# Performance work log

Hardware: AMD Instinct MI355X
Metric: run time of the kernel (lower is better)

The kernel has to match this reference:

```python
import jax, jax.numpy as jnp
import numpy as np

D_MODEL = 512
STATE = 128
HALF = STATE // 2
SEQ = 4096
BATCH = 8


def setup_inputs() -> dict:
    key = jax.random.key(0)
    ks = jax.random.split(key, 4)
    u = jax.random.normal(ks[0], (BATCH, SEQ, D_MODEL), dtype=jnp.float32)
    # HiPPO init: Lambda = -0.5 + i*pi*n, n=1..HALF
    n = jnp.arange(1, HALF + 1, dtype=jnp.float32)
    log_Lambda_real = jnp.log(jnp.full((HALF,), 0.5, dtype=jnp.float32))  # log(-real) with real=-0.5
    Lambda_imag = jnp.pi * n
    B_real = jnp.ones((HALF, D_MODEL), dtype=jnp.float32)
    B_imag = jnp.zeros((HALF, D_MODEL), dtype=jnp.float32)
    C_real = jax.random.normal(ks[1], (D_MODEL, HALF), dtype=jnp.float32) / np.sqrt(STATE)
    C_imag = jax.random.normal(ks[2], (D_MODEL, HALF), dtype=jnp.float32) / np.sqrt(STATE)
    D = jax.random.normal(ks[3], (D_MODEL, D_MODEL), dtype=jnp.float32) / np.sqrt(D_MODEL)
    log_Delta = jnp.array([-3.0], dtype=jnp.float32)
    return {
        "u": u,
        "log_Lambda_real": log_Lambda_real,
        "Lambda_imag": Lambda_imag,
        "B_real": B_real,
        "B_imag": B_imag,
        "C_real": C_real,
        "C_imag": C_imag,
        "D": D,
        "log_Delta": log_Delta,
    }


def reference(u, log_Lambda_real, Lambda_imag, B_real, B_imag, C_real, C_imag, D, log_Delta):
    T = u.shape[1]
    Bc = B_real + 1j * B_imag            # (N/2, P) complex
    Cc = C_real + 1j * C_imag            # (P, N/2) complex
    # --- bilinear (Tustin) discretization ---
    Delta = jnp.exp(log_Delta)           # (1,)
    Lambda = -jnp.exp(jnp.clip(log_Lambda_real, -10.0, 10.0)) + 1j * Lambda_imag  # (N/2,)
    denom = 1.0 - (Delta / 2.0) * Lambda
    A_bar = (1.0 + (Delta / 2.0) * Lambda) / denom          # (N/2,)
    B_bar = (Delta / denom)[:, None] * Bc                   # (N/2, P)
    # --- FFT convolution with the SSM kernel k[n,t] = A_bar[n]^t ---
    t_idx = jnp.arange(T)
    k = jnp.exp(jnp.log(A_bar)[:, None] * t_idx[None, :])   # (N/2, T)
    u_c = u.astype(jnp.complex64)
    v = jnp.einsum('np,btp->bnt', B_bar, u_c)               # (B, N/2, T)
    fft_size = 2 * T
    V_f = jnp.fft.fft(v, n=fft_size, axis=-1)
    K_f = jnp.fft.fft(k, n=fft_size, axis=-1)
    conv = jnp.fft.ifft(V_f * K_f[None, :, :], axis=-1)[..., :T]  # (B, N/2, T)
    y = 2.0 * jnp.einsum('pn,bnt->btp', Cc, conv).real      # (B, T, P)
    return y + u @ D.T
```

## Files before the change

### kernel.cpp

```cpp
#include <hip/hip_runtime.h>
#include <hip/hip_bf16.h>
#include <stdint.h>


#define BATCH 8
#define SEQ   4096
#define DMODEL 512
#define HALF  64
#define CHUNK 64
#define NCHUNK (SEQ / CHUNK)
#define NT    10

typedef __attribute__((ext_vector_type(8))) short short8;
typedef __attribute__((ext_vector_type(4))) float f32x4;

__device__ __forceinline__ unsigned short f2bf(float f) {
    unsigned int u = __float_as_uint(f);
    u += 0x7fffu + ((u >> 16) & 1u);
    return (unsigned short)(u >> 16);
}
__device__ __forceinline__ float bf2f(unsigned short s) {
    return __uint_as_float((unsigned)s << 16);
}

__device__ __forceinline__ void poleA(const float* logLr, const float* Li_in,
                                      const float* logDelta, int n,
                                      float& Ar, float& Ai) {
    float Delta = expf(logDelta[0]);
    float llr = fminf(fmaxf(logLr[n], -10.f), 10.f);
    float Lr = -expf(llr);
    float Li = Li_in[n];
    float dr = 1.f - 0.5f * Delta * Lr;
    float di = -0.5f * Delta * Li;
    float dn = dr * dr + di * di;
    float nr = 1.f + 0.5f * Delta * Lr;
    float ni = 0.5f * Delta * Li;
    Ar = (nr * dr + ni * di) / dn;
    Ai = (ni * dr - nr * di) / dn;
}

#define GLOAD_LDS16(g, l)                                                    \
    __builtin_amdgcn_global_load_lds(                                        \
        (const __attribute__((address_space(1))) unsigned int*)(g),          \
        (__attribute__((address_space(3))) unsigned int*)(l), 16, 0, 0)

__global__ void k_build(const float* __restrict__ logLr, const float* __restrict__ Li_in,
                        const float* __restrict__ logDelta,
                        const float* __restrict__ Br, const float* __restrict__ Bi,
                        const float* __restrict__ Cr, const float* __restrict__ Ci,
                        const float* __restrict__ D,
                        unsigned short* __restrict__ Mv, unsigned short* __restrict__ W) {
    int bid = blockIdx.x;
    if (bid < 128) {
        int np = bid, p = threadIdx.x;
        if (p < DMODEL) {
            int n = np & 63;
            float Delta = expf(logDelta[0]);
            float llr = fminf(fmaxf(logLr[n], -10.f), 10.f);
            float Lr = -expf(llr);
            float Li = Li_in[n];
            float dr = 1.f - 0.5f * Delta * Lr;
            float di = -0.5f * Delta * Li;
            float dn = dr * dr + di * di;
            float sr = Delta * dr / dn;
            float si = -Delta * di / dn;
            float br = Br[n * DMODEL + p], bi = Bi[n * DMODEL + p];
            float v = (np < HALF) ? (sr * br - si * bi) : (si * br + sr * bi);
            Mv[np * DMODEL + p] = f2bf(v);
        }
    } else {
        int p = bid - 128, j = threadIdx.x;
        float v;
        if (j < HALF) v = 2.f * Cr[p * HALF + j];
        else if (j < 2 * HALF) v = -2.f * Ci[p * HALF + (j - HALF)];
        else v = D[p * DMODEL + (j - 2 * HALF)];
        W[p * 640 + j] = f2bf(v);
    }
}

__global__ void k_scanA(const unsigned short* __restrict__ Vb,
                        const float* __restrict__ logLr, const float* __restrict__ Li_in,
                        const float* __restrict__ logDelta,
                        float* __restrict__ E) {
    int tid = threadIdx.x;
    int n = tid & 63;
    int c = ((blockIdx.x & 31) << 1) + (tid >> 6);
    int b = blockIdx.x >> 5;
    float Ar, Ai;
    poleA(logLr, Li_in, logDelta, n, Ar, Ai);
    float xr = 0.f, xi = 0.f;
    size_t base = ((size_t)b * SEQ + (size_t)c * CHUNK) * 128 + n;
    for (int tl = 0; tl < CHUNK; ++tl) {
        float vr = bf2f(Vb[base]), vi = bf2f(Vb[base + 64]);
        float nxr = Ar * xr - Ai * xi + vr;
        float nxi = Ar * xi + Ai * xr + vi;
        xr = nxr; xi = nxi;
        base += 128;
    }
    int eidx = ((b * NCHUNK + c) * 2) * HALF + n;
    E[eidx] = xr; E[eidx + 64] = xi;
}

__global__ void k_scanCB(const unsigned short* __restrict__ Vb,
                         const float* __restrict__ E,
                         const float* __restrict__ logLr, const float* __restrict__ Li_in,
                         const float* __restrict__ logDelta,
                         unsigned short* __restrict__ Xb) {
    int tid = threadIdx.x;
    int n = tid & 63;
    int c = ((blockIdx.x & 31) << 1) + (tid >> 6);
    int b = blockIdx.x >> 5;
    float Ar, Ai;
    poleA(logLr, Li_in, logDelta, n, Ar, Ai);
    float a64r = Ar, a64i = Ai;
#pragma unroll
    for (int s = 0; s < 6; ++s) {
        float t = a64r * a64r - a64i * a64i;
        a64i = 2.f * a64r * a64i;
        a64r = t;
    }
    float xr = 0.f, xi = 0.f, wr = 1.f, wi = 0.f;
    for (int jj = 1; jj <= c; ++jj) {
        int ei = ((b * NCHUNK + (c - jj)) * 2) * HALF + n;
        float er = E[ei], ev = E[ei + 64];
        xr += wr * er - wi * ev;
        xi += wr * ev + wi * er;
        float nwr = wr * a64r - wi * a64i;
        float nwi = wr * a64i + wi * a64r;
        wr = nwr; wi = nwi;
    }
    size_t base = ((size_t)b * SEQ + (size_t)c * CHUNK) * 128 + n;
    for (int tl = 0; tl < CHUNK; ++tl) {
        float vr = bf2f(Vb[base]), vi = bf2f(Vb[base + 64]);
        float nxr = Ar * xr - Ai * xi + vr;
        float nxi = Ar * xi + Ai * xr + vi;
        xr = nxr; xi = nxi;
        Xb[base] = f2bf(xr); Xb[base + 64] = f2bf(xi);
        base += 128;
    }
}

__global__ __launch_bounds__(512) void gemm1(const float* __restrict__ U,
                                             const unsigned short* __restrict__ Mv,
                                             unsigned short* __restrict__ Vb,
                                             unsigned short* __restrict__ Ub) {
    __shared__ __align__(16) unsigned short As[64 * 32];
    __shared__ __align__(16) unsigned short Bs[128 * 32];
    const int tid = threadIdx.x;
    const int lane = tid & 63;
    const int w = tid >> 6;
    const int wm = w >> 2, wn = w & 3;
    const int l15 = lane & 15, l4 = lane >> 4;
    const int row0 = blockIdx.x * 64;
    const int srow = tid >> 3;
    const int sh = (tid & 7) * 4;

    f32x4 acc[2][2];
#pragma unroll
    for (int m = 0; m < 2; ++m)
#pragma unroll
        for (int n = 0; n < 2; ++n) acc[m][n] = (f32x4)(0.f);

    for (int k0 = 0; k0 < DMODEL; k0 += 32) {
        const float4 av = *(const float4*)(U + (size_t)(row0 + srow) * DMODEL + k0 + sh);

        __syncthreads();

        GLOAD_LDS16(Mv + (size_t)(tid >> 2) * DMODEL + k0 + (tid & 3) * 8,
                    &Bs[(w * 64) * 8]);

        uint2 wa;
        wa.x = (unsigned)f2bf(av.x) | ((unsigned)f2bf(av.y) << 16);
        wa.y = (unsigned)f2bf(av.z) | ((unsigned)f2bf(av.w) << 16);
        *(uint2*)&As[srow * 32 + sh] = wa;
        *(uint2*)&Ub[(size_t)(row0 + srow) * DMODEL + k0 + sh] = wa;

        __syncthreads();

        short8 af[2], bf[2];
#pragma unroll
        for (int m = 0; m < 2; ++m)
            af[m] = *(const short8*)&As[(wm * 32 + m * 16 + l15) * 32 + l4 * 8];
#pragma unroll
        for (int n = 0; n < 2; ++n)
            bf[n] = *(const short8*)&Bs[(wn * 32 + n * 16 + l15) * 32 + l4 * 8];
#pragma unroll
        for (int m = 0; m < 2; ++m)
#pragma unroll
            for (int n = 0; n < 2; ++n)
                acc[m][n] = __builtin_amdgcn_mfma_f32_16x16x32_bf16(af[m], bf[n], acc[m][n], 0, 0, 0);
    }

#pragma unroll
    for (int m = 0; m < 2; ++m) {
        int rbase = row0 + wm * 32 + m * 16 + l4 * 4;
#pragma unroll
        for (int n = 0; n < 2; ++n) {
            int col = wn * 32 + n * 16 + l15;
#pragma unroll
            for (int r = 0; r < 4; ++r)
                Vb[(size_t)(rbase + r) * 128 + col] = f2bf(acc[m][n][r]);
        }
    }
}


#define STAGE_K(t, kh, j) do {                                                 \
    int c_ = (kh) * 1024 + (j) * 512 + tid;                                    \
    int ct_ = c_ ^ (((c_ >> 5) & 1) << 1);                                     \
    int r_ = (ct_ >> 2) & 255;                                                 \
    int kcol_ = (t) * 64 + (kh) * 32 + (ct_ & 3) * 8;                          \
    const unsigned short* asrc_ = (kcol_ < 128)                                \
        ? Xb + (size_t)(row0 + r_) * 128 + kcol_                               \
        : Ub + (size_t)(row0 + r_) * 512 + (kcol_ - 128);                      \
    GLOAD_LDS16(asrc_, &As[((t) & 1) * 16384 + ((kh) * 1024 + (j) * 512 + w * 64) * 8]); \
    GLOAD_LDS16(W + (size_t)(col0 + r_) * 640 + kcol_,                         \
                &Bs[((t) & 1) * 16384 + ((kh) * 1024 + (j) * 512 + w * 64) * 8]); \
} while (0)

#define LDAB(t, kh) do {                                                       \
    _Pragma("unroll") for (int i_ = 0; i_ < 8; ++i_) {                         \
        int r_ = wm * 128 + i_ * 16 + l15;                                     \
        int c_ = (l4 * 8) ^ (((r_ >> 3) & 1) << 4);                            \
        af[i_] = *(const short8*)&As[((t) & 1) * 16384 + (kh) * 8192 + r_ * 32 + c_]; \
    }                                                                          \
    _Pragma("unroll") for (int j_ = 0; j_ < 4; ++j_) {                         \
        int r_ = wn * 64 + j_ * 16 + l15;                                      \
        int c_ = (l4 * 8) ^ (((r_ >> 3) & 1) << 4);                            \
        bf[j_] = *(const short8*)&Bs[((t) & 1) * 16384 + (kh) * 8192 + r_ * 32 + c_]; \
    } } while (0)

#define MFMA32() do {                                                          \
    __builtin_amdgcn_s_setprio(1);                                             \
    _Pragma("unroll") for (int i_ = 0; i_ < 8; ++i_)                           \
    _Pragma("unroll") for (int j_ = 0; j_ < 4; ++j_)                           \
        acc[i_][j_] = __builtin_amdgcn_mfma_f32_16x16x32_bf16(                 \
            bf[j_], af[i_], acc[i_][j_], 0, 0, 0);                             \
    __builtin_amdgcn_s_setprio(0);                                             \
} while (0)

#define PHASE_SYNC(N) do {                                                     \
    asm volatile("s_waitcnt vmcnt(" #N ")" ::: "memory");                      \
    __builtin_amdgcn_s_barrier();                                              \
    __builtin_amdgcn_sched_barrier(0);                                         \
} while (0)

__global__ __launch_bounds__(512) void gemm23_8p(const unsigned short* __restrict__ Xb,
                                                 const unsigned short* __restrict__ Ub,
                                                 const unsigned short* __restrict__ W,
                                                 float* __restrict__ C) {
    __shared__ __align__(16) unsigned short As[2 * 16384];
    __shared__ __align__(16) unsigned short Bs[2 * 16384];
    const int tid = threadIdx.x;
    const int lane = tid & 63;
    const int w = tid >> 6;
    const int wm = w >> 2, wn = w & 3;
    const int l15 = lane & 15, l4 = lane >> 4;

    int lin = blockIdx.y * gridDim.x + blockIdx.x;
    int sw = (lin & 7) * 32 + (lin >> 3);
    const int row0 = (sw & 127) * 256;
    const int col0 = (sw >> 7) * 256;

    f32x4 acc[8][4];
#pragma unroll
    for (int m = 0; m < 8; ++m)
#pragma unroll
        for (int n = 0; n < 4; ++n) acc[m][n] = (f32x4)(0.f);

    STAGE_K(0, 0, 0); STAGE_K(0, 0, 1);
    STAGE_K(0, 1, 0); STAGE_K(0, 1, 1);
    STAGE_K(1, 0, 0); STAGE_K(1, 0, 1);

    short8 af[8], bf[4];
    for (int t = 0; t < NT - 1; ++t) {
        PHASE_SYNC(8);
        LDAB(t, 0);
        STAGE_K(t + 1, 1, 0); STAGE_K(t + 1, 1, 1);
        MFMA32();
        PHASE_SYNC(8);
        LDAB(t, 1);
        if (t < NT - 2) { STAGE_K(t + 2, 0, 0); STAGE_K(t + 2, 0, 1); }
        MFMA32();
    }
    PHASE_SYNC(4);
    LDAB(NT - 1, 0);
    MFMA32();
    PHASE_SYNC(0);
    LDAB(NT - 1, 1);
    MFMA32();

#pragma unroll
    for (int i = 0; i < 8; ++i) {
        int row = row0 + wm * 128 + i * 16 + l15;
#pragma unroll
        for (int j = 0; j < 4; ++j) {
            int col = col0 + wn * 64 + j * 16 + l4 * 4;
            *(float4*)&C[(size_t)row * DMODEL + col] =
                make_float4(acc[i][j][0], acc[i][j][1], acc[i][j][2], acc[i][j][3]);
        }
    }
}


extern "C" void kernel_launch(void* const* d_in, const int* in_sizes, int n_in,
                              void* d_out, int out_size, void* d_ws, size_t ws_size,
                              hipStream_t stream) {
    const float* u      = (const float*)d_in[0];
    const float* logLr  = (const float*)d_in[1];
    const float* Li     = (const float*)d_in[2];
    const float* Br     = (const float*)d_in[3];
    const float* Bi     = (const float*)d_in[4];
    const float* Cr     = (const float*)d_in[5];
    const float* Ci     = (const float*)d_in[6];
    const float* D      = (const float*)d_in[7];
    const float* logDel = (const float*)d_in[8];
    float* out = (float*)d_out;

    const size_t M = (size_t)BATCH * SEQ;
    unsigned short* Vb = (unsigned short*)d_ws;
    unsigned short* Ub = Vb + M * 128;
    unsigned short* Xb = Ub + M * 512;
    unsigned short* Mv = Xb + M * 128;
    unsigned short* W  = Mv + 128 * 512;
    float* E     = (float*)(W + 512 * 640);

    hipLaunchKernelGGL(k_build, dim3(640), dim3(640), 0, stream,
                       logLr, Li, logDel, Br, Bi, Cr, Ci, D, Mv, W);

    hipLaunchKernelGGL(gemm1, dim3(M / 64), dim3(512), 0, stream, u, Mv, Vb, Ub);

    hipLaunchKernelGGL(k_scanA, dim3(256), dim3(128), 0, stream,
                       Vb, logLr, Li, logDel, E);
    hipLaunchKernelGGL(k_scanCB, dim3(256), dim3(128), 0, stream,
                       Vb, E, logLr, Li, logDel, Xb);

    hipLaunchKernelGGL(gemm23_8p, dim3(M / 256, DMODEL / 256), dim3(512), 0, stream,
                       Xb, Ub, W, out);
}
```

Measured before the change: 79.82 us.

## Fuse chunk-end scan state computation into gemm1 epilogue

Removes the separate k_scanA kernel. The per-chunk final state is now computed inside gemm1's epilogue as a weighted sum of the fp32 accumulators times powers of the pole A (A^(63-t)), reduced with wave shuffles and shared memory. This saves one kernel launch and a full sequential re-read of Vb. The trade is extra epilogue math, a block sync in gemm1, and a closed-form power sum in place of the sequential recurrence, which may shift rounding (it now uses fp32 accumulators rather than bf16 Vb).

New measurement: 78.24 us, median of 3. -2.0%, faster.

```diff
diff --git a/kernel.cpp b/kernel.cpp
--- a/kernel.cpp
+++ b/kernel.cpp
@@ -37,6 +37,18 @@
     float ni = 0.5f * Delta * Li;
     Ar = (nr * dr + ni * di) / dn;
     Ai = (ni * dr - nr * di) / dn;
+}
+
+__device__ __forceinline__ void cpow(float Ar, float Ai, int e,
+                                     float& wr, float& wi) {
+    wr = 1.f; wi = 0.f;
+    float br = Ar, bi = Ai;
+#pragma unroll
+    for (int k = 0; k < 6; ++k) {
+        if (e & 1) { float t = wr * br - wi * bi; wi = wr * bi + wi * br; wr = t; }
+        float t2 = br * br - bi * bi; bi = 2.f * br * bi; br = t2;
+        e >>= 1;
+    }
 }
 
 #define GLOAD_LDS16(g, l)                                                    \
@@ -78,29 +90,6 @@
     }
 }
 
-__global__ void k_scanA(const unsigned short* __restrict__ Vb,
-                        const float* __restrict__ logLr, const float* __restrict__ Li_in,
-                        const float* __restrict__ logDelta,
-                        float* __restrict__ E) {
-    int tid = threadIdx.x;
-    int n = tid & 63;
-    int c = ((blockIdx.x & 31) << 1) + (tid >> 6);
-    int b = blockIdx.x >> 5;
-    float Ar, Ai;
-    poleA(logLr, Li_in, logDelta, n, Ar, Ai);
-    float xr = 0.f, xi = 0.f;
-    size_t base = ((size_t)b * SEQ + (size_t)c * CHUNK) * 128 + n;
-    for (int tl = 0; tl < CHUNK; ++tl) {
-        float vr = bf2f(Vb[base]), vi = bf2f(Vb[base + 64]);
-        float nxr = Ar * xr - Ai * xi + vr;
-        float nxi = Ar * xi + Ai * xr + vi;
-        xr = nxr; xi = nxi;
-        base += 128;
-    }
-    int eidx = ((b * NCHUNK + c) * 2) * HALF + n;
-    E[eidx] = xr; E[eidx + 64] = xi;
-}
-
 __global__ void k_scanCB(const unsigned short* __restrict__ Vb,
                          const float* __restrict__ E,
                          const float* __restrict__ logLr, const float* __restrict__ Li_in,
@@ -143,9 +132,14 @@
 __global__ __launch_bounds__(512) void gemm1(const float* __restrict__ U,
                                              const unsigned short* __restrict__ Mv,
                                              unsigned short* __restrict__ Vb,
-                                             unsigned short* __restrict__ Ub) {
+                                             unsigned short* __restrict__ Ub,
+                                             const float* __restrict__ logLr,
+                                             const float* __restrict__ Li_in,
+                                             const float* __restrict__ logDelta,
+                                             float* __restrict__ E) {
     __shared__ __align__(16) unsigned short As[64 * 32];
     __shared__ __align__(16) unsigned short Bs[128 * 32];
+    __shared__ float Ered[8][2][16][2];
     const int tid = threadIdx.x;
     const int lane = tid & 63;
     const int w = tid >> 6;
@@ -201,6 +195,62 @@
             for (int r = 0; r < 4; ++r)
                 Vb[(size_t)(rbase + r) * 128 + col] = f2bf(acc[m][n][r]);
         }
+    }
+
+    {
+        const int base = wm * 32 + l4 * 4;
+        const int isIm = (wn >= 2);
+#pragma unroll
+        for (int nf = 0; nf < 2; ++nf) {
+            int pole = ((wn & 1) * 32) + nf * 16 + l15;
+            float Ar, Ai;
+            poleA(logLr, Li_in, logDelta, pole, Ar, Ai);
+            float a2r = Ar * Ar - Ai * Ai, a2i = 2.f * Ar * Ai;
+            float a4r = a2r * a2r - a2i * a2i, a4i = 2.f * a2r * a2i;
+            float a8r = a4r * a4r - a4i * a4i, a8i = 2.f * a4r * a4i;
+            float a12r = a8r * a4r - a8i * a4i, a12i = a8r * a4i + a8i * a4r;
+            float wr, wi;
+            cpow(Ar, Ai, 44 - base, wr, wi);
+            float s2re = 0.f, s2im = 0.f;
+#pragma unroll
+            for (int m = 1; m >= 0; --m) {
+#pragma unroll
+                for (int r = 3; r >= 0; --r) {
+                    float v = acc[m][nf][r];
+                    if (isIm) { s2re -= wi * v; s2im += wr * v; }
+                    else      { s2re += wr * v; s2im += wi * v; }
+                    float nwr = wr * Ar - wi * Ai;
+                    float nwi = wr * Ai + wi * Ar;
+                    wr = nwr; wi = nwi;
+                }
+                if (m == 1) {
+                    float nwr = wr * a12r - wi * a12i;
+                    float nwi = wr * a12i + wi * a12r;
+                    wr = nwr; wi = nwi;
+                }
+            }
+            s2re += __shfl_xor(s2re, 16, 64);
+            s2re += __shfl_xor(s2re, 32, 64);
+            s2im += __shfl_xor(s2im, 16, 64);
+            s2im += __shfl_xor(s2im, 32, 64);
+            if (l4 == 0) {
+                Ered[w][nf][l15][0] = s2re;
+                Ered[w][nf][l15][1] = s2im;
+            }
+        }
+    }
+    __syncthreads();
+    if (tid < 128) {
+        int p = tid & 63;
+        int comp = tid >> 6;
+        int wn1 = p >> 5;
+        int nf = (p >> 4) & 1;
+        int l = p & 15;
+        float s = Ered[0 * 4 + wn1][nf][l][comp] + Ered[0 * 4 + wn1 + 2][nf][l][comp]
+                + Ered[1 * 4 + wn1][nf][l][comp] + Ered[1 * 4 + wn1 + 2][nf][l][comp];
+        int b = row0 >> 12;
+        int c = (row0 >> 6) & 63;
+        E[((b * NCHUNK + c) * 2) * HALF + comp * 64 + p] = s;
     }
 }
 
@@ -328,10 +378,9 @@
     hipLaunchKernelGGL(k_build, dim3(640), dim3(640), 0, stream,
                        logLr, Li, logDel, Br, Bi, Cr, Ci, D, Mv, W);
 
-    hipLaunchKernelGGL(gemm1, dim3(M / 64), dim3(512), 0, stream, u, Mv, Vb, Ub);
-
-    hipLaunchKernelGGL(k_scanA, dim3(256), dim3(128), 0, stream,
-                       Vb, logLr, Li, logDel, E);
+    hipLaunchKernelGGL(gemm1, dim3(M / 64), dim3(512), 0, stream,
+                       u, Mv, Vb, Ub, logLr, Li, logDel, E);
+
     hipLaunchKernelGGL(k_scanCB, dim3(256), dim3(128), 0, stream,
                        Vb, E, logLr, Li, logDel, Xb);
 
```
